# Kernel optimization log

Measured on AMD Instinct MI355X. Metric: run time of the kernel, lower is better.

## Reference

```python
import jax, jax.numpy as jnp
import numpy as np

N = 20000      # nodes
E = 320000     # edges (before self loops)
F_IN = 256     # num_node_features
H = 8          # heads
C = 64         # dim_h per head
B = 64         # graphs in batch
NC = 10        # num_classes
HID = H * C    # 512


def setup_inputs() -> dict:
    key = jax.random.key(0)
    ks = jax.random.split(key, 20)
    def glorot(k, shape, fan):
        return jax.random.normal(k, shape, jnp.float32) / np.sqrt(fan)
    inp = {
        'x': jax.random.normal(ks[0], (N, F_IN), jnp.float32),
        'edge_index': jax.random.randint(ks[1], (2, E), 0, N),
        'batch': jnp.sort(jax.random.randint(ks[2], (N,), 0, B)),
        # conv1: F_IN -> H*C
        'W1': glorot(ks[3], (F_IN, HID), F_IN),
        'a_src1': glorot(ks[4], (H, C), C),
        'a_dst1': glorot(ks[5], (H, C), C),
        'b1': jnp.zeros((HID,), jnp.float32),
        # conv2: HID -> H*C
        'W2': glorot(ks[6], (HID, HID), HID),
        'a_src2': glorot(ks[7], (H, C), C),
        'a_dst2': glorot(ks[8], (H, C), C),
        'b2': jnp.zeros((HID,), jnp.float32),
        # conv3: HID -> H*C
        'W3': glorot(ks[9], (HID, HID), HID),
        'a_src3': glorot(ks[10], (H, C), C),
        'a_dst3': glorot(ks[11], (H, C), C),
        'b3': jnp.zeros((HID,), jnp.float32),
        # final classifier
        'Wl': glorot(ks[12], (HID, NC), HID),
        'bl': jnp.zeros((NC,), jnp.float32),
    }
    return inp


def _gat_conv(x, src, dst, W, a_src, a_dst, b):
    """PyG GATConv (concat=True, negative_slope=0.2). src/dst include self loops."""
    xt = (x @ W).reshape(-1, H, C)                      # [N, H, C]
    al_s = jnp.einsum('nhc,hc->nh', xt, a_src)          # [N, H]
    al_d = jnp.einsum('nhc,hc->nh', xt, a_dst)
    e = jax.nn.leaky_relu(al_s[src] + al_d[dst], 0.2)   # [E', H]
    m = jax.ops.segment_max(e, dst, num_segments=N)     # segment softmax (stable)
    m = jax.lax.stop_gradient(jnp.where(jnp.isfinite(m), m, 0.0))
    p = jnp.exp(e - m[dst])
    s = jax.ops.segment_sum(p, dst, num_segments=N)
    alpha = p / (s[dst] + 1e-16)                        # [E', H]
    msg = xt[src] * alpha[..., None]                    # [E', H, C]
    out = jax.ops.segment_sum(msg, dst, num_segments=N) # [N, H, C]
    return out.reshape(-1, HID) + b


def reference(x, edge_index, batch, W1, a_src1, a_dst1, b1,
              W2, a_src2, a_dst2, b2, W3, a_src3, a_dst3, b3, Wl, bl):
    loop = jnp.arange(N, dtype=edge_index.dtype)
    src = jnp.concatenate([edge_index[0], loop])        # add_self_loops=True
    dst = jnp.concatenate([edge_index[1], loop])

    h = jax.nn.elu(_gat_conv(x, src, dst, W1, a_src1, a_dst1, b1))
    h = jax.nn.elu(_gat_conv(h, src, dst, W2, a_src2, a_dst2, b2))
    h = jax.nn.elu(_gat_conv(h, src, dst, W3, a_src3, a_dst3, b3))

    # global mean pool over graphs
    cnt = jax.ops.segment_sum(jnp.ones((N,), h.dtype), batch, num_segments=B)
    hG = jax.ops.segment_sum(h, batch, num_segments=B) / jnp.clip(cnt, 1.0)[:, None]

    # dropout p=0.5 is identity in eval mode
    logits = hG @ Wl + bl
    return hG, jax.nn.softmax(logits, axis=1)
```

## Files before the change

### kernel.cpp

```cpp
#include <hip/hip_runtime.h>
#include <hip/hip_bf16.h>
#include <math.h>

#define N_NODES  20000
#define E_EDGES  320000
#define E_TOT    (E_EDGES + N_NODES)
#define F_INF    256
#define HEADS    8
#define CDIM     64
#define HID      512
#define B_GRAPHS 64
#define NCLS     10
#define M_PAD    20096
#define NSCAN    20
#define NWG_GEMM 1256

typedef __attribute__((ext_vector_type(8))) short short8;
typedef __attribute__((ext_vector_type(4))) float f32x4;

__device__ inline unsigned short f2bf(float x) {
    unsigned u = __builtin_bit_cast(unsigned, x);
    u += 0x7fff + ((u >> 16) & 1);
    return (unsigned short)(u >> 16);
}
__device__ inline float bf2f(unsigned short h) {
    unsigned u = ((unsigned)h) << 16;
    return __builtin_bit_cast(float, u);
}

#define GLOAD_LDS16(g, l) __builtin_amdgcn_global_load_lds(                     \
        (const __attribute__((address_space(1))) void*)(g),                     \
        (__attribute__((address_space(3))) void*)(l), 16, 0, 0)

__global__ __launch_bounds__(256) void zero_ints(int* p, int n) {
    int i = blockIdx.x * 256 + threadIdx.x;
    if (i < n) p[i] = 0;
}

__global__ __launch_bounds__(256) void zero_pad_rows(unsigned short* hi, unsigned short* lo) {
    int i = blockIdx.x * 256 + threadIdx.x;
    const int tot = (M_PAD - N_NODES) * HID;
    if (i < tot) {
        hi[(size_t)N_NODES * HID + i] = 0;
        lo[(size_t)N_NODES * HID + i] = 0;
    }
}

__global__ __launch_bounds__(256) void split_pad(const float* __restrict__ src,
                                                 unsigned short* __restrict__ hi,
                                                 unsigned short* __restrict__ lo,
                                                 int M, int K, long total) {
    long i = ((long)blockIdx.x * 256 + threadIdx.x) * 4;
    if (i >= total) return;
    int row = (int)(i / K);
    float4 v = make_float4(0.f, 0.f, 0.f, 0.f);
    if (row < M) v = *(const float4*)(src + i);
    ushort4 h, l;
    h.x = f2bf(v.x); l.x = f2bf(v.x - bf2f(h.x));
    h.y = f2bf(v.y); l.y = f2bf(v.y - bf2f(h.y));
    h.z = f2bf(v.z); l.z = f2bf(v.z - bf2f(h.z));
    h.w = f2bf(v.w); l.w = f2bf(v.w - bf2f(h.w));
    *(ushort4*)(hi + i) = h;
    *(ushort4*)(lo + i) = l;
}

__global__ __launch_bounds__(256) void transpose_split_B(const float* __restrict__ B,
                                                         unsigned short* __restrict__ Bthi,
                                                         unsigned short* __restrict__ Btlo,
                                                         int K) {
    __shared__ float t[32][33];
    int n0 = blockIdx.x * 32, k0 = blockIdx.y * 32;
    int tx = threadIdx.x & 31, ty = threadIdx.x >> 5;
    for (int i = ty; i < 32; i += 8) t[i][tx] = B[(size_t)(k0 + i) * HID + n0 + tx];
    __syncthreads();
    for (int i = ty; i < 32; i += 8) {
        float v = t[tx][i];
        unsigned short h = f2bf(v);
        unsigned short l = f2bf(v - bf2f(h));
        Bthi[(size_t)(n0 + i) * K + k0 + tx] = h;
        Btlo[(size_t)(n0 + i) * K + k0 + tx] = l;
    }
}

__global__ __launch_bounds__(256) void gemm_mfma(const unsigned short* __restrict__ Ahi,
                                                 const unsigned short* __restrict__ Alo,
                                                 const unsigned short* __restrict__ Bhi,
                                                 const unsigned short* __restrict__ Blo,
                                                 const float* __restrict__ a_src,
                                                 const float* __restrict__ a_dst,
                                                 unsigned short* __restrict__ xtb,
                                                 float* __restrict__ al_s,
                                                 float* __restrict__ al_d,
                                                 int M, int K) {
    __shared__ short AsHi[4096], AsLo[4096], BsHi[2048], BsLo[2048];
    const int tid = threadIdx.x;
    const int w = tid >> 6, lane = tid & 63;

    const int xcd = blockIdx.x & 7, idx = blockIdx.x >> 3;
    const int wg = xcd * (NWG_GEMM >> 3) + idx;
    const int row0 = (wg >> 3) * 128, col0 = (wg & 7) * 64;

    long offA[2];
    int ldsA[2];
#pragma unroll
    for (int i = 0; i < 2; ++i) {
        int u = w * 128 + i * 64 + lane;
        int row = u >> 2;
        int kg = (u & 3) ^ ((row >> 1) & 3);
        offA[i] = ((long)(row0 + row) * K + kg * 8) * 2;
        ldsA[i] = (w * 128 + i * 64) * 8;
    }
    long offB;
    int ldsB;
    {
        int u = w * 64 + lane;
        int row = u >> 2;
        int kg = (u & 3) ^ ((row >> 1) & 3);
        offB = ((long)(col0 + row) * K + kg * 8) * 2;
        ldsB = (w * 64) * 8;
    }

    const int r16 = lane & 15, kg = lane >> 4;
    int aOff[2], bOff[4];
#pragma unroll
    for (int i = 0; i < 2; ++i) {
        int row = w * 32 + i * 16 + r16;
        aOff[i] = (row * 4 + (kg ^ ((row >> 1) & 3))) * 16;
    }
#pragma unroll
    for (int j = 0; j < 4; ++j) {
        int col = j * 16 + r16;
        bOff[j] = (col * 4 + (kg ^ ((col >> 1) & 3))) * 16;
    }

    const char* pAhi = (const char*)Ahi;
    const char* pAlo = (const char*)Alo;
    const char* pBhi = (const char*)Bhi;
    const char* pBlo = (const char*)Blo;

    f32x4 acc[2][4] = {};

    for (int kk = 0; kk < K; kk += 32) {
        long kb = (long)kk * 2;
        __syncthreads();
#pragma unroll
        for (int i = 0; i < 2; ++i) {
            GLOAD_LDS16(pAhi + offA[i] + kb, AsHi + ldsA[i]);
            GLOAD_LDS16(pAlo + offA[i] + kb, AsLo + ldsA[i]);
        }
        GLOAD_LDS16(pBhi + offB + kb, BsHi + ldsB);
        GLOAD_LDS16(pBlo + offB + kb, BsLo + ldsB);
        __syncthreads();

        short8 fah[2], fal[2], fbh[4], fbl[4];
#pragma unroll
        for (int i = 0; i < 2; ++i) {
            fah[i] = *(const short8*)((const char*)AsHi + aOff[i]);
            fal[i] = *(const short8*)((const char*)AsLo + aOff[i]);
        }
#pragma unroll
        for (int j = 0; j < 4; ++j) {
            fbh[j] = *(const short8*)((const char*)BsHi + bOff[j]);
            fbl[j] = *(const short8*)((const char*)BsLo + bOff[j]);
        }
#pragma unroll
        for (int i = 0; i < 2; ++i)
#pragma unroll
            for (int j = 0; j < 4; ++j) {
                acc[i][j] = __builtin_amdgcn_mfma_f32_16x16x32_bf16(fah[i], fbh[j], acc[i][j], 0, 0, 0);
                acc[i][j] = __builtin_amdgcn_mfma_f32_16x16x32_bf16(fah[i], fbl[j], acc[i][j], 0, 0, 0);
                acc[i][j] = __builtin_amdgcn_mfma_f32_16x16x32_bf16(fal[i], fbh[j], acc[i][j], 0, 0, 0);
            }
    }

    const int h = col0 >> 6;
    float asv[4], adv[4];
#pragma unroll
    for (int j = 0; j < 4; ++j) {
        asv[j] = a_src[h * CDIM + j * 16 + r16];
        adv[j] = a_dst[h * CDIM + j * 16 + r16];
    }
#pragma unroll
    for (int i = 0; i < 2; ++i) {
        int rbase = row0 + w * 32 + i * 16 + (lane >> 4) * 4;
#pragma unroll
        for (int rr = 0; rr < 4; ++rr) {
            float ss = acc[i][0][rr] * asv[0] + acc[i][1][rr] * asv[1]
                     + acc[i][2][rr] * asv[2] + acc[i][3][rr] * asv[3];
            float dd = acc[i][0][rr] * adv[0] + acc[i][1][rr] * adv[1]
                     + acc[i][2][rr] * adv[2] + acc[i][3][rr] * adv[3];
#pragma unroll
            for (int off = 1; off < 16; off <<= 1) {
                ss += __shfl_xor(ss, off);
                dd += __shfl_xor(dd, off);
            }
            int row = rbase + rr;
            if ((lane & 15) == 0 && row < M) {
                al_s[row * HEADS + h] = ss;
                al_d[row * HEADS + h] = dd;
            }
        }
#pragma unroll
        for (int j = 0; j < 4; ++j) {
            int col = col0 + j * 16 + r16;
#pragma unroll
            for (int rr = 0; rr < 4; ++rr)
                if (rbase + rr < M) xtb[(size_t)(rbase + rr) * HID + col] = f2bf(acc[i][j][rr]);
        }
    }
}

__global__ __launch_bounds__(256) void count_edges(const int* __restrict__ ei,
                                                   int* __restrict__ counts) {
    int e = blockIdx.x * 256 + threadIdx.x;
    if (e < E_TOT) {
        int dst = (e < E_EDGES) ? ei[E_EDGES + e] : (e - E_EDGES);
        atomicAdd(&counts[dst], 1);
    }
}

__global__ __launch_bounds__(1024) void scan_local(const int* __restrict__ counts,
                                                   int* __restrict__ incl,
                                                   int* __restrict__ bsum) {
    __shared__ int s[1024];
    int tid = threadIdx.x;
    int i = blockIdx.x * 1024 + tid;
    int v = (i < N_NODES) ? counts[i] : 0;
    s[tid] = v;
    __syncthreads();
    for (int off = 1; off < 1024; off <<= 1) {
        int t = (tid >= off) ? s[tid - off] : 0;
        __syncthreads();
        s[tid] += t;
        __syncthreads();
    }
    if (i < N_NODES) incl[i] = s[tid];
    if (tid == 1023) bsum[blockIdx.x] = s[1023];
}

__global__ __launch_bounds__(64) void scan_bsums(const int* __restrict__ bsum,
                                                 int* __restrict__ bpre) {
    int lane = threadIdx.x;
    int v = (lane < NSCAN) ? bsum[lane] : 0;
    int incl = v;
#pragma unroll
    for (int off = 1; off < 32; off <<= 1) {
        int t = __shfl_up(incl, off);
        if (lane >= off) incl += t;
    }
    if (lane < NSCAN) bpre[lane] = incl - v;
}

__global__ __launch_bounds__(1024) void scan_finalize(const int* __restrict__ counts,
                                                      const int* __restrict__ incl,
                                                      const int* __restrict__ bpre,
                                                      int* __restrict__ offsets,
                                                      int* __restrict__ cursor) {
    int i = blockIdx.x * 1024 + threadIdx.x;
    if (i < N_NODES) {
        int inc = incl[i] + bpre[blockIdx.x];
        offsets[i + 1] = inc;
        cursor[i] = inc - counts[i];
    }
    if (i == 0) offsets[0] = 0;
}

__global__ __launch_bounds__(256) void scatter_edges(const int* __restrict__ ei,
                                                     int* __restrict__ cursor,
                                                     int* __restrict__ csr) {
    int e = blockIdx.x * 256 + threadIdx.x;
    if (e < E_TOT) {
        int srcn, dst;
        if (e < E_EDGES) { srcn = ei[e]; dst = ei[E_EDGES + e]; }
        else             { srcn = dst = e - E_EDGES; }
        int pos = atomicAdd(&cursor[dst], 1);
        csr[pos] = srcn;
    }
}

__global__ __launch_bounds__(256) void gat_aggregate4(const unsigned short* __restrict__ xtb,
                                                      const float* __restrict__ al_s,
                                                      const float* __restrict__ al_d,
                                                      const int* __restrict__ offsets,
                                                      const int* __restrict__ csr,
                                                      const float* __restrict__ bias,
                                                      unsigned short* __restrict__ outHi,
                                                      unsigned short* __restrict__ outLo) {
    const int lane = threadIdx.x & 63;
    const int n = blockIdx.x * 4 + (threadIdx.x >> 6);
    const int h = lane >> 3;
    const int c0 = lane * 8;
    const int beg = offsets[n];
    const int deg = offsets[n + 1] - beg;
    const float aldv = al_d[n * HEADS + h];

    float acc[8] = {};
    float psum = 0.f;

#pragma unroll 4
    for (int i = 0; i < deg; ++i) {
        int srcn = csr[beg + i];
        float ev = al_s[srcn * HEADS + h] + aldv;
        ev = (ev >= 0.f) ? ev : 0.2f * ev;
        float p = __expf(ev);
        psum += p;
        short8 row = *(const short8*)(xtb + (size_t)srcn * HID + c0);
#pragma unroll
        for (int j = 0; j < 8; ++j)
            acc[j] = fmaf(p, bf2f((unsigned short)row[j]), acc[j]);
    }

    const float inv = 1.f / (psum + 1e-16f);
    float4 b0 = *(const float4*)(bias + c0);
    float4 b1 = *(const float4*)(bias + c0 + 4);
    float bv[8] = { b0.x, b0.y, b0.z, b0.w, b1.x, b1.y, b1.z, b1.w };
    short8 h8, l8;
#pragma unroll
    for (int j = 0; j < 8; ++j) {
        float v = acc[j] * inv + bv[j];
        v = (v > 0.f) ? v : expm1f(v);
        unsigned short hi = f2bf(v);
        h8[j] = (short)hi;
        l8[j] = (short)f2bf(v - bf2f(hi));
    }
    size_t o = (size_t)n * HID + c0;
    *(short8*)(outHi + o) = h8;
    *(short8*)(outLo + o) = l8;
}

__global__ __launch_bounds__(128) void find_bounds(const int* __restrict__ batch,
                                                   int* __restrict__ bounds) {
    int b = threadIdx.x;
    if (b <= B_GRAPHS) {
        int lo = 0, hi = N_NODES;
        while (lo < hi) {
            int mid = (lo + hi) >> 1;
            if (batch[mid] < b) lo = mid + 1; else hi = mid;
        }
        bounds[b] = lo;
    }
}

__global__ __launch_bounds__(256) void pool_partial(const unsigned short* __restrict__ hHi,
                                                    const unsigned short* __restrict__ hLo,
                                                    const int* __restrict__ bounds,
                                                    float* __restrict__ partial) {
    const int b = blockIdx.x, y = blockIdx.y, k = blockIdx.z;
    const int s = bounds[b], cnt = bounds[b + 1] - s;
    const int ns = s + (cnt * k) / 4;
    const int ne = s + (cnt * (k + 1)) / 4;
    const int t = threadIdx.x;
    const int chp = t & 31;
    const int nl = t >> 5;

    float a0 = 0.f, a1 = 0.f;
    for (int n = ns + nl; n < ne; n += 8) {
        size_t off = (size_t)n * HID + y * 64 + chp * 2;
        unsigned vh = *(const unsigned*)(hHi + off);
        unsigned vl = *(const unsigned*)(hLo + off);
        a0 += bf2f((unsigned short)(vh & 0xffff)) + bf2f((unsigned short)(vl & 0xffff));
        a1 += bf2f((unsigned short)(vh >> 16)) + bf2f((unsigned short)(vl >> 16));
    }
    __shared__ float red[4][32][2];
    a0 += __shfl_xor(a0, 32);
    a1 += __shfl_xor(a1, 32);
    if ((t & 63) < 32) { red[t >> 6][chp][0] = a0; red[t >> 6][chp][1] = a1; }
    __syncthreads();
    if (t < 64) {
        int cp = t >> 1, c = t & 1;
        float v = red[0][cp][c] + red[1][cp][c] + red[2][cp][c] + red[3][cp][c];
        partial[(((size_t)k * B_GRAPHS + b) * 8 + y) * 64 + cp * 2 + c] = v;
    }
}

__global__ __launch_bounds__(512) void pool_final(const float* __restrict__ partial,
                                                  const int* __restrict__ bounds,
                                                  float* __restrict__ hG) {
    const int b = blockIdx.x, t = threadIdx.x;
    float v = 0.f;
#pragma unroll
    for (int k = 0; k < 4; ++k)
        v += partial[((size_t)k * B_GRAPHS + b) * HID + t];
    float cnt = fmaxf((float)(bounds[b + 1] - bounds[b]), 1.0f);
    hG[b * HID + t] = v / cnt;
}

__global__ __launch_bounds__(64) void classifier_kernel(const float* __restrict__ hG,
                                                        const float* __restrict__ Wl,
                                                        const float* __restrict__ bl,
                                                        float* __restrict__ outP) {
    int b = blockIdx.x;
    int tid = threadIdx.x;
    __shared__ float row[HID];
    __shared__ float logit[NCLS];
    for (int j = tid; j < HID; j += 64) row[j] = hG[b * HID + j];
    __syncthreads();
    if (tid < NCLS) {
        float acc = bl[tid];
        for (int j = 0; j < HID; ++j) acc += row[j] * Wl[j * NCLS + tid];
        logit[tid] = acc;
    }
    __syncthreads();
    if (tid == 0) {
        float mx = logit[0];
        for (int k = 1; k < NCLS; ++k) mx = fmaxf(mx, logit[k]);
        float ssum = 0.f, ex[NCLS];
        for (int k = 0; k < NCLS; ++k) { ex[k] = expf(logit[k] - mx); ssum += ex[k]; }
        for (int k = 0; k < NCLS; ++k) outP[b * NCLS + k] = ex[k] / ssum;
    }
}

extern "C" void kernel_launch(void* const* d_in, const int* in_sizes, int n_in,
                              void* d_out, int out_size, void* d_ws, size_t ws_size,
                              hipStream_t stream) {
    const float* x     = (const float*)d_in[0];
    const int*   ei    = (const int*)d_in[1];
    const int*   batch = (const int*)d_in[2];
    const float* W[3]  = { (const float*)d_in[3], (const float*)d_in[7],  (const float*)d_in[11] };
    const float* as_[3] = { (const float*)d_in[4], (const float*)d_in[8],  (const float*)d_in[12] };
    const float* ad_[3] = { (const float*)d_in[5], (const float*)d_in[9],  (const float*)d_in[13] };
    const float* bb[3] = { (const float*)d_in[6], (const float*)d_in[10], (const float*)d_in[14] };
    const float* Wl    = (const float*)d_in[15];
    const float* bl    = (const float*)d_in[16];

    char* ws = (char*)d_ws;
    unsigned short* A1hi = (unsigned short*)ws;      ws += (size_t)M_PAD * F_INF * 2;
    unsigned short* A1lo = (unsigned short*)ws;      ws += (size_t)M_PAD * F_INF * 2;
    unsigned short* A2hi = (unsigned short*)ws;      ws += (size_t)M_PAD * HID * 2;
    unsigned short* A2lo = (unsigned short*)ws;      ws += (size_t)M_PAD * HID * 2;
    unsigned short* Bthi = (unsigned short*)ws;      ws += (size_t)HID * HID * 2;
    unsigned short* Btlo = (unsigned short*)ws;      ws += (size_t)HID * HID * 2;
    unsigned short* xtb  = (unsigned short*)ws;      ws += (size_t)N_NODES * HID * 2;
    float* als  = (float*)ws;                        ws += (size_t)N_NODES * HEADS * 4;
    float* ald  = (float*)ws;                        ws += (size_t)N_NODES * HEADS * 4;
    float* partial = (float*)ws;                     ws += (size_t)4 * B_GRAPHS * HID * 4;
    int* counts  = (int*)ws;                         ws += (size_t)N_NODES * 4;
    int* incl    = (int*)ws;                         ws += (size_t)N_NODES * 4;
    int* bsum    = (int*)ws;                         ws += 32 * 4;
    int* bpre    = (int*)ws;                         ws += 32 * 4;
    int* offsets = (int*)ws;                         ws += (size_t)(N_NODES + 1) * 4;
    int* cursor  = (int*)ws;                         ws += (size_t)N_NODES * 4;
    int* csr     = (int*)ws;                         ws += (size_t)E_TOT * 4;
    int* bounds  = (int*)ws;                         ws += (size_t)(B_GRAPHS + 1) * 4;

    float* hG = (float*)d_out;
    float* probs = (float*)d_out + (size_t)B_GRAPHS * HID;

    zero_ints<<<(N_NODES + 255) / 256, 256, 0, stream>>>(counts, N_NODES);
    count_edges<<<(E_TOT + 255) / 256, 256, 0, stream>>>(ei, counts);
    scan_local<<<NSCAN, 1024, 0, stream>>>(counts, incl, bsum);
    scan_bsums<<<1, 64, 0, stream>>>(bsum, bpre);
    scan_finalize<<<NSCAN, 1024, 0, stream>>>(counts, incl, bpre, offsets, cursor);
    scatter_edges<<<(E_TOT + 255) / 256, 256, 0, stream>>>(ei, cursor, csr);
    find_bounds<<<1, 128, 0, stream>>>(batch, bounds);
    zero_pad_rows<<<((M_PAD - N_NODES) * HID + 255) / 256, 256, 0, stream>>>(A2hi, A2lo);

    {
        long totA = (long)M_PAD * F_INF;
        split_pad<<<(int)(totA / 4 / 256), 256, 0, stream>>>(x, A1hi, A1lo, N_NODES, F_INF, totA);
        transpose_split_B<<<dim3(HID / 32, F_INF / 32), 256, 0, stream>>>(W[0], Bthi, Btlo, F_INF);
        gemm_mfma<<<NWG_GEMM, 256, 0, stream>>>(A1hi, A1lo, Bthi, Btlo, as_[0], ad_[0],
                                                xtb, als, ald, N_NODES, F_INF);
        gat_aggregate4<<<N_NODES / 4, 256, 0, stream>>>(xtb, als, ald, offsets, csr, bb[0], A2hi, A2lo);
    }

    for (int L = 1; L < 3; ++L) {
        transpose_split_B<<<dim3(HID / 32, HID / 32), 256, 0, stream>>>(W[L], Bthi, Btlo, HID);
        gemm_mfma<<<NWG_GEMM, 256, 0, stream>>>(A2hi, A2lo, Bthi, Btlo, as_[L], ad_[L],
                                                xtb, als, ald, N_NODES, HID);
        gat_aggregate4<<<N_NODES / 4, 256, 0, stream>>>(xtb, als, ald, offsets, csr, bb[L], A2hi, A2lo);
    }

    {
        dim3 pgrid(B_GRAPHS, 8, 4);
        pool_partial<<<pgrid, 256, 0, stream>>>(A2hi, A2lo, bounds, partial);
        pool_final<<<B_GRAPHS, 512, 0, stream>>>(partial, bounds, hG);
    }
    classifier_kernel<<<B_GRAPHS, 64, 0, stream>>>(hG, Wl, bl, probs);
}
```

Baseline: 384.0 us.

## Fuse small setup kernels, use memsets, and aggregate two nodes per wavefront

Merges the batch-bounds search into scan_local, folds the block-sum prefix into scan_finalize, fuses pooling finalisation with the classifier, and replaces two zeroing kernels with hipMemsetAsync. The aggregation kernel now processes two destination nodes per wavefront with interleaved edge loops, giving more independent loads in flight. The goal is fewer kernel launches and more memory-level parallelism in the gather. The cost is divergence when the two nodes have different degrees, and a serial loop in scan_finalize.

```diff
diff --git a/kernel.cpp b/kernel.cpp
--- a/kernel.cpp
+++ b/kernel.cpp
@@ -31,20 +31,6 @@
 #define GLOAD_LDS16(g, l) __builtin_amdgcn_global_load_lds(                     \
         (const __attribute__((address_space(1))) void*)(g),                     \
         (__attribute__((address_space(3))) void*)(l), 16, 0, 0)
-
-__global__ __launch_bounds__(256) void zero_ints(int* p, int n) {
-    int i = blockIdx.x * 256 + threadIdx.x;
-    if (i < n) p[i] = 0;
-}
-
-__global__ __launch_bounds__(256) void zero_pad_rows(unsigned short* hi, unsigned short* lo) {
-    int i = blockIdx.x * 256 + threadIdx.x;
-    const int tot = (M_PAD - N_NODES) * HID;
-    if (i < tot) {
-        hi[(size_t)N_NODES * HID + i] = 0;
-        lo[(size_t)N_NODES * HID + i] = 0;
-    }
-}
 
 __global__ __launch_bounds__(256) void split_pad(const float* __restrict__ src,
                                                  unsigned short* __restrict__ hi,
@@ -221,10 +207,20 @@
 
 __global__ __launch_bounds__(1024) void scan_local(const int* __restrict__ counts,
                                                    int* __restrict__ incl,
-                                                   int* __restrict__ bsum) {
+                                                   int* __restrict__ bsum,
+                                                   const int* __restrict__ batch,
+                                                   int* __restrict__ bounds) {
     __shared__ int s[1024];
     int tid = threadIdx.x;
     int i = blockIdx.x * 1024 + tid;
+    if (blockIdx.x == 0 && tid <= B_GRAPHS) {
+        int lo = 0, hi = N_NODES;
+        while (lo < hi) {
+            int mid = (lo + hi) >> 1;
+            if (batch[mid] < tid) lo = mid + 1; else hi = mid;
+        }
+        bounds[tid] = lo;
+    }
     int v = (i < N_NODES) ? counts[i] : 0;
     s[tid] = v;
     __syncthreads();
@@ -238,27 +234,21 @@
     if (tid == 1023) bsum[blockIdx.x] = s[1023];
 }
 
-__global__ __launch_bounds__(64) void scan_bsums(const int* __restrict__ bsum,
-                                                 int* __restrict__ bpre) {
-    int lane = threadIdx.x;
-    int v = (lane < NSCAN) ? bsum[lane] : 0;
-    int incl = v;
-#pragma unroll
-    for (int off = 1; off < 32; off <<= 1) {
-        int t = __shfl_up(incl, off);
-        if (lane >= off) incl += t;
-    }
-    if (lane < NSCAN) bpre[lane] = incl - v;
-}
-
 __global__ __launch_bounds__(1024) void scan_finalize(const int* __restrict__ counts,
                                                       const int* __restrict__ incl,
-                                                      const int* __restrict__ bpre,
+                                                      const int* __restrict__ bsum,
                                                       int* __restrict__ offsets,
                                                       int* __restrict__ cursor) {
+    __shared__ int bpre_s;
+    if (threadIdx.x == 0) {
+        int s = 0;
+        for (int j = 0; j < blockIdx.x; ++j) s += bsum[j];
+        bpre_s = s;
+    }
+    __syncthreads();
     int i = blockIdx.x * 1024 + threadIdx.x;
     if (i < N_NODES) {
-        int inc = incl[i] + bpre[blockIdx.x];
+        int inc = incl[i] + bpre_s;
         offsets[i + 1] = inc;
         cursor[i] = inc - counts[i];
     }
@@ -278,7 +268,7 @@
     }
 }
 
-__global__ __launch_bounds__(256) void gat_aggregate4(const unsigned short* __restrict__ xtb,
+__global__ __launch_bounds__(256) void gat_aggregate5(const unsigned short* __restrict__ xtb,
                                                       const float* __restrict__ al_s,
                                                       const float* __restrict__ al_d,
                                                       const int* __restrict__ offsets,
@@ -287,58 +277,73 @@
                                                       unsigned short* __restrict__ outHi,
                                                       unsigned short* __restrict__ outLo) {
     const int lane = threadIdx.x & 63;
-    const int n = blockIdx.x * 4 + (threadIdx.x >> 6);
+    const int n0 = blockIdx.x * 8 + (threadIdx.x >> 6) * 2;
+    const int n1 = n0 + 1;
     const int h = lane >> 3;
     const int c0 = lane * 8;
-    const int beg = offsets[n];
-    const int deg = offsets[n + 1] - beg;
-    const float aldv = al_d[n * HEADS + h];
-
-    float acc[8] = {};
-    float psum = 0.f;
-
-#pragma unroll 4
-    for (int i = 0; i < deg; ++i) {
-        int srcn = csr[beg + i];
-        float ev = al_s[srcn * HEADS + h] + aldv;
-        ev = (ev >= 0.f) ? ev : 0.2f * ev;
-        float p = __expf(ev);
-        psum += p;
-        short8 row = *(const short8*)(xtb + (size_t)srcn * HID + c0);
-#pragma unroll
-        for (int j = 0; j < 8; ++j)
-            acc[j] = fmaf(p, bf2f((unsigned short)row[j]), acc[j]);
-    }
-
-    const float inv = 1.f / (psum + 1e-16f);
+    const int beg0 = offsets[n0], deg0 = offsets[n0 + 1] - beg0;
+    const int beg1 = offsets[n1], deg1 = offsets[n1 + 1] - beg1;
+    const float ald0 = al_d[n0 * HEADS + h];
+    const float ald1 = al_d[n1 * HEADS + h];
+
+    float acc0[8] = {}, acc1[8] = {};
+    float ps0 = 0.f, ps1 = 0.f;
+    const int dm = max(deg0, deg1);
+
+    for (int i = 0; i < dm; ++i) {
+        if (i < deg0) {
+            int s = csr[beg0 + i];
+            float ev = al_s[s * HEADS + h] + ald0;
+            ev = (ev >= 0.f) ? ev : 0.2f * ev;
+            float p = __expf(ev);
+            ps0 += p;
+            short8 row = *(const short8*)(xtb + (size_t)s * HID + c0);
+#pragma unroll
+            for (int j = 0; j < 8; ++j)
+                acc0[j] = fmaf(p, bf2f((unsigned short)row[j]), acc0[j]);
+        }
+        if (i < deg1) {
+            int s = csr[beg1 + i];
+            float ev = al_s[s * HEADS + h] + ald1;
+            ev = (ev >= 0.f) ? ev : 0.2f * ev;
+            float p = __expf(ev);
+            ps1 += p;
+            short8 row = *(const short8*)(xtb + (size_t)s * HID + c0);
+#pragma unroll
+            for (int j = 0; j < 8; ++j)
+                acc1[j] = fmaf(p, bf2f((unsigned short)row[j]), acc1[j]);
+        }
+    }
+
     float4 b0 = *(const float4*)(bias + c0);
     float4 b1 = *(const float4*)(bias + c0 + 4);
     float bv[8] = { b0.x, b0.y, b0.z, b0.w, b1.x, b1.y, b1.z, b1.w };
+
+    const float inv0 = 1.f / (ps0 + 1e-16f);
+    const float inv1 = 1.f / (ps1 + 1e-16f);
     short8 h8, l8;
 #pragma unroll
     for (int j = 0; j < 8; ++j) {
-        float v = acc[j] * inv + bv[j];
+        float v = acc0[j] * inv0 + bv[j];
         v = (v > 0.f) ? v : expm1f(v);
         unsigned short hi = f2bf(v);
         h8[j] = (short)hi;
         l8[j] = (short)f2bf(v - bf2f(hi));
     }
-    size_t o = (size_t)n * HID + c0;
-    *(short8*)(outHi + o) = h8;
-    *(short8*)(outLo + o) = l8;
-}
-
-__global__ __launch_bounds__(128) void find_bounds(const int* __restrict__ batch,
-                                                   int* __restrict__ bounds) {
-    int b = threadIdx.x;
-    if (b <= B_GRAPHS) {
-        int lo = 0, hi = N_NODES;
-        while (lo < hi) {
-            int mid = (lo + hi) >> 1;
-            if (batch[mid] < b) lo = mid + 1; else hi = mid;
-        }
-        bounds[b] = lo;
-    }
+    size_t o0 = (size_t)n0 * HID + c0;
+    *(short8*)(outHi + o0) = h8;
+    *(short8*)(outLo + o0) = l8;
+#pragma unroll
+    for (int j = 0; j < 8; ++j) {
+        float v = acc1[j] * inv1 + bv[j];
+        v = (v > 0.f) ? v : expm1f(v);
+        unsigned short hi = f2bf(v);
+        h8[j] = (short)hi;
+        l8[j] = (short)f2bf(v - bf2f(hi));
+    }
+    size_t o1 = (size_t)n1 * HID + c0;
+    *(short8*)(outHi + o1) = h8;
+    *(short8*)(outLo + o1) = l8;
 }
 
 __global__ __launch_bounds__(256) void pool_partial(const unsigned short* __restrict__ hHi,
@@ -373,35 +378,31 @@
     }
 }
 
-__global__ __launch_bounds__(512) void pool_final(const float* __restrict__ partial,
-                                                  const int* __restrict__ bounds,
-                                                  float* __restrict__ hG) {
+__global__ __launch_bounds__(512) void pool_classify(const float* __restrict__ partial,
+                                                     const int* __restrict__ bounds,
+                                                     const float* __restrict__ Wl,
+                                                     const float* __restrict__ bl,
+                                                     float* __restrict__ hG,
+                                                     float* __restrict__ outP) {
     const int b = blockIdx.x, t = threadIdx.x;
+    __shared__ float row[HID];
+    __shared__ float logit[NCLS];
     float v = 0.f;
 #pragma unroll
     for (int k = 0; k < 4; ++k)
         v += partial[((size_t)k * B_GRAPHS + b) * HID + t];
     float cnt = fmaxf((float)(bounds[b + 1] - bounds[b]), 1.0f);
-    hG[b * HID + t] = v / cnt;
-}
-
-__global__ __launch_bounds__(64) void classifier_kernel(const float* __restrict__ hG,
-                                                        const float* __restrict__ Wl,
-                                                        const float* __restrict__ bl,
-                                                        float* __restrict__ outP) {
-    int b = blockIdx.x;
-    int tid = threadIdx.x;
-    __shared__ float row[HID];
-    __shared__ float logit[NCLS];
-    for (int j = tid; j < HID; j += 64) row[j] = hG[b * HID + j];
-    __syncthreads();
-    if (tid < NCLS) {
-        float acc = bl[tid];
-        for (int j = 0; j < HID; ++j) acc += row[j] * Wl[j * NCLS + tid];
-        logit[tid] = acc;
-    }
-    __syncthreads();
-    if (tid == 0) {
+    v /= cnt;
+    hG[b * HID + t] = v;
+    row[t] = v;
+    __syncthreads();
+    if (t < NCLS) {
+        float acc = bl[t];
+        for (int j = 0; j < HID; ++j) acc += row[j] * Wl[j * NCLS + t];
+        logit[t] = acc;
+    }
+    __syncthreads();
+    if (t == 0) {
         float mx = logit[0];
         for (int k = 1; k < NCLS; ++k) mx = fmaxf(mx, logit[k]);
         float ssum = 0.f, ex[NCLS];
@@ -437,7 +438,6 @@
     int* counts  = (int*)ws;                         ws += (size_t)N_NODES * 4;
     int* incl    = (int*)ws;                         ws += (size_t)N_NODES * 4;
     int* bsum    = (int*)ws;                         ws += 32 * 4;
-    int* bpre    = (int*)ws;                         ws += 32 * 4;
     int* offsets = (int*)ws;                         ws += (size_t)(N_NODES + 1) * 4;
     int* cursor  = (int*)ws;                         ws += (size_t)N_NODES * 4;
     int* csr     = (int*)ws;                         ws += (size_t)E_TOT * 4;
@@ -446,14 +446,13 @@
     float* hG = (float*)d_out;
     float* probs = (float*)d_out + (size_t)B_GRAPHS * HID;
 
-    zero_ints<<<(N_NODES + 255) / 256, 256, 0, stream>>>(counts, N_NODES);
+    hipMemsetAsync(counts, 0, (size_t)N_NODES * 4, stream);
     count_edges<<<(E_TOT + 255) / 256, 256, 0, stream>>>(ei, counts);
-    scan_local<<<NSCAN, 1024, 0, stream>>>(counts, incl, bsum);
-    scan_bsums<<<1, 64, 0, stream>>>(bsum, bpre);
-    scan_finalize<<<NSCAN, 1024, 0, stream>>>(counts, incl, bpre, offsets, cursor);
+    scan_local<<<NSCAN, 1024, 0, stream>>>(counts, incl, bsum, batch, bounds);
+    scan_finalize<<<NSCAN, 1024, 0, stream>>>(counts, incl, bsum, offsets, cursor);
     scatter_edges<<<(E_TOT + 255) / 256, 256, 0, stream>>>(ei, cursor, csr);
-    find_bounds<<<1, 128, 0, stream>>>(batch, bounds);
-    zero_pad_rows<<<((M_PAD - N_NODES) * HID + 255) / 256, 256, 0, stream>>>(A2hi, A2lo);
+    hipMemsetAsync(A2hi + (size_t)N_NODES * HID, 0, (size_t)(M_PAD - N_NODES) * HID * 2, stream);
+    hipMemsetAsync(A2lo + (size_t)N_NODES * HID, 0, (size_t)(M_PAD - N_NODES) * HID * 2, stream);
 
     {
         long totA = (long)M_PAD * F_INF;
@@ -461,20 +460,19 @@
         transpose_split_B<<<dim3(HID / 32, F_INF / 32), 256, 0, stream>>>(W[0], Bthi, Btlo, F_INF);
         gemm_mfma<<<NWG_GEMM, 256, 0, stream>>>(A1hi, A1lo, Bthi, Btlo, as_[0], ad_[0],
                                                 xtb, als, ald, N_NODES, F_INF);
-        gat_aggregate4<<<N_NODES / 4, 256, 0, stream>>>(xtb, als, ald, offsets, csr, bb[0], A2hi, A2lo);
+        gat_aggregate5<<<N_NODES / 8, 256, 0, stream>>>(xtb, als, ald, offsets, csr, bb[0], A2hi, A2lo);
     }
 
     for (int L = 1; L < 3; ++L) {
         transpose_split_B<<<dim3(HID / 32, HID / 32), 256, 0, stream>>>(W[L], Bthi, Btlo, HID);
         gemm_mfma<<<NWG_GEMM, 256, 0, stream>>>(A2hi, A2lo, Bthi, Btlo, as_[L], ad_[L],
                                                 xtb, als, ald, N_NODES, HID);
-        gat_aggregate4<<<N_NODES / 4, 256, 0, stream>>>(xtb, als, ald, offsets, csr, bb[L], A2hi, A2lo);
+        gat_aggregate5<<<N_NODES / 8, 256, 0, stream>>>(xtb, als, ald, offsets, csr, bb[L], A2hi, A2lo);
     }
 
     {
         dim3 pgrid(B_GRAPHS, 8, 4);
         pool_partial<<<pgrid, 256, 0, stream>>>(A2hi, A2lo, bounds, partial);
-        pool_final<<<B_GRAPHS, 512, 0, stream>>>(partial, bounds, hG);
-    }
-    classifier_kernel<<<B_GRAPHS, 64, 0, stream>>>(hG, Wl, bl, probs);
-}
+        pool_classify<<<B_GRAPHS, 512, 0, stream>>>(partial, bounds, Wl, bl, hG, probs);
+    }
+}
```

Result: slower. 435.6 us (+13.4%).
